# Optimization experiments

Measured on AMD Instinct MI355X. Metric: run time of the kernel, lower is better.

Reference implementation:

```python
import jax, jax.numpy as jnp
import numpy as np

N = 4096
DIMS = {"word": 768, "pos": 64, "liwc": 93, "entity": 256, "text": 768}
HID, OUT = 256, 128
VIEWS = ["word", "pos", "liwc", "entity", "text"]


def setup_inputs() -> dict:
    key = jax.random.key(0)
    inp = {}
    for i, v in enumerate(VIEWS):
        ka, kx, k1, k2 = jax.random.split(jax.random.fold_in(key, i), 4)
        d = DIMS[v]
        # dense row-normalized adjacency surrogate
        a = jax.random.uniform(ka, (N, N), dtype=jnp.float32)
        inp[f"adj_{v}"] = a / jnp.sum(a, axis=1, keepdims=True)
        inp[f"x_{v}"] = jax.random.normal(kx, (N, d), dtype=jnp.float32)
        inp[f"W1_{v}"] = jax.random.normal(k1, (d, HID), dtype=jnp.float32) * (2.0 / (d + HID)) ** 0.5
        inp[f"b1_{v}"] = jnp.zeros((HID,), dtype=jnp.float32)
        inp[f"W2_{v}"] = jax.random.normal(k2, (HID, OUT), dtype=jnp.float32) * (2.0 / (HID + OUT)) ** 0.5
        inp[f"b2_{v}"] = jnp.zeros((OUT,), dtype=jnp.float32)
    return inp


def _gcn2(adj, x, W1, b1, W2, b2):
    # layer 1: adj @ (x @ W1) + b1, relu (dropout is identity in eval mode)
    h = jax.nn.relu(adj @ (x @ W1) + b1)
    # layer 2
    return adj @ (h @ W2) + b2


def reference(adj_word, adj_pos, adj_liwc, adj_entity, adj_text,
              x_word, x_pos, x_liwc, x_entity, x_text,
              W1_word, b1_word, W2_word, b2_word,
              W1_pos, b1_pos, W2_pos, b2_pos,
              W1_liwc, b1_liwc, W2_liwc, b2_liwc,
              W1_entity, b1_entity, W2_entity, b2_entity,
              W1_text, b1_text, W2_text, b2_text):
    return (
        _gcn2(adj_word, x_word, W1_word, b1_word, W2_word, b2_word),
        _gcn2(adj_pos, x_pos, W1_pos, b1_pos, W2_pos, b2_pos),
        _gcn2(adj_liwc, x_liwc, W1_liwc, b1_liwc, W2_liwc, b2_liwc),
        _gcn2(adj_entity, x_entity, W1_entity, b1_entity, W2_entity, b2_entity),
        _gcn2(adj_text, x_text, W1_text, b1_text, W2_text, b2_text),
    )
```

## Files before the change

kernel.cpp:

```cpp
#include <hip/hip_runtime.h>
#include <stdint.h>

typedef unsigned short u16;
typedef __attribute__((ext_vector_type(8))) __bf16 bf16x8;
typedef __attribute__((ext_vector_type(4))) float f32x4;
typedef __attribute__((ext_vector_type(4))) u16 u16x4;
typedef __attribute__((ext_vector_type(8))) u16 u16x8;

#define BM 128
#define BN 128
#define BK 32
#define MTOT 4096

__device__ __forceinline__ u16 f2bf(float f) {
  union { float f; uint32_t u; } x; x.f = f;
  uint32_t r = x.u + 0x7FFFu + ((x.u >> 16) & 1u);
  return (u16)(r >> 16);
}
__device__ __forceinline__ float bf2f(u16 h) {
  union { uint32_t u; float f; } x; x.u = ((uint32_t)h) << 16;
  return x.f;
}

__device__ __forceinline__ void gload16(const void* g, void* lds) {
  __builtin_amdgcn_global_load_lds(
      (const __attribute__((address_space(1))) void*)g,
      (__attribute__((address_space(3))) void*)lds, 16, 0, 0);
}

struct ViewParams {
  const void* A;
  const u16* BT;
  void* C;
  const float* bias;
  int ldab, lda, N;
  int kspan;
  size_t partStride;
};
struct Params5 { ViewParams v[5]; };

template <int FLAGS, bool AF32, bool CF32>
__global__ __launch_bounds__(256) void gemm_kernel(Params5 p, int tilesPerView,
                                                   int ntiles, int kchunks) {
  constexpr int ABYTES = AF32 ? (BM * BK * 4) : (BM * BK * 2);
  constexpr int BUFB = ABYTES + BN * BK * 2;
  __shared__ __align__(16) char smem[2 * BUFB];

  const int bid = blockIdx.x;
  const int view = bid / tilesPerView;
  const int t = bid - view * tilesPerView;
  const int kc = t % kchunks;
  const int t2 = t / kchunks;
  const int nt = t2 % ntiles;
  const int mt = t2 / ntiles;
  ViewParams vp = p.v[view];
  const int ldab = vp.ldab, lda = vp.lda, N = vp.N;
  const int m0 = mt * BM, n0 = nt * BN;
  const int kbase = kc * vp.kspan;

  const int tid = threadIdx.x;
  const int wave = tid >> 6;
  const int lane = tid & 63;

  const int srow = lane >> 2;
  const int slot4 = lane & 3;
  const int rB0 = wave * 32 + srow;
  const int rB1 = rB0 + 16;
  const int cB0 = slot4 ^ ((rB0 >> 1) & 3);
  const int cB1 = slot4 ^ ((rB1 >> 1) & 3);
  const u16* gB0 = vp.BT + (size_t)(n0 + rB0) * ldab + kbase + cB0 * 8;
  const u16* gB1 = vp.BT + (size_t)(n0 + rB1) * ldab + kbase + cB1 * 8;
  const int lB0_off = ABYTES + (wave * 32) * 32 * 2;
  const int lB1_off = ABYTES + (wave * 32 + 16) * 32 * 2;

  const float* gAf[4];
  const u16 *gAb0 = nullptr, *gAb1 = nullptr;
  int lA_off[4];
  if constexpr (AF32) {
    const float* Af = (const float*)vp.A;
    const int arow = lane >> 3;
    const int slot8 = lane & 7;
#pragma unroll
    for (int i = 0; i < 4; i++) {
      int r = wave * 32 + i * 8 + arow;
      int c = slot8 ^ (r & 7);
      gAf[i] = Af + (size_t)(m0 + r) * lda + kbase + c * 4;
      lA_off[i] = (wave * 32 + i * 8) * 32 * 4;
    }
  } else {
    const u16* Ab = (const u16*)vp.A;
    const int rA0 = wave * 32 + srow;
    const int rA1 = rA0 + 16;
    const int cA0 = slot4 ^ ((rA0 >> 1) & 3);
    const int cA1 = slot4 ^ ((rA1 >> 1) & 3);
    gAb0 = Ab + (size_t)(m0 + rA0) * lda + kbase + cA0 * 8;
    gAb1 = Ab + (size_t)(m0 + rA1) * lda + kbase + cA1 * 8;
    lA_off[0] = (wave * 32) * 32 * 2;
    lA_off[1] = (wave * 32 + 16) * 32 * 2;
  }

  const int lm = lane & 15;
  const int q = lane >> 4;
  const int wm = (wave >> 1) * 64;
  const int wn = (wave & 1) * 64;
  int aoff0[4], aoff1[4], boff[4];
#pragma unroll
  for (int i = 0; i < 4; i++) {
    int ml = wm + i * 16 + lm;
    if constexpr (AF32) {
      aoff0[i] = ml * 32 + ((2 * q) ^ (ml & 7)) * 4;
      aoff1[i] = ml * 32 + ((2 * q + 1) ^ (ml & 7)) * 4;
    } else {
      aoff0[i] = ml * 32 + (q ^ ((ml >> 1) & 3)) * 8;
    }
    int nl = wn + i * 16 + lm;
    boff[i] = nl * 32 + (q ^ ((nl >> 1) & 3)) * 8;
  }

  f32x4 acc[4][4];
#pragma unroll
  for (int i = 0; i < 4; i++)
#pragma unroll
    for (int j = 0; j < 4; j++) acc[i][j] = 0.0f;

  auto stage = [&](char* bufp) {
    if constexpr (AF32) {
#pragma unroll
      for (int i = 0; i < 4; i++) { gload16(gAf[i], bufp + lA_off[i]); gAf[i] += BK; }
    } else {
      gload16(gAb0, bufp + lA_off[0]);
      gload16(gAb1, bufp + lA_off[1]);
      gAb0 += BK; gAb1 += BK;
    }
    gload16(gB0, bufp + lB0_off);
    gload16(gB1, bufp + lB1_off);
    gB0 += BK; gB1 += BK;
  };

  auto compute = [&](const char* bufp) {
    bf16x8 af[4], bfr[4];
#pragma unroll
    for (int i = 0; i < 4; i++) {
      if constexpr (AF32) {
        f32x4 lo = *(const f32x4*)((const float*)bufp + aoff0[i]);
        f32x4 hi = *(const f32x4*)((const float*)bufp + aoff1[i]);
        bf16x8 a;
#pragma unroll
        for (int tt = 0; tt < 4; tt++) { a[tt] = (__bf16)lo[tt]; a[tt + 4] = (__bf16)hi[tt]; }
        af[i] = a;
      } else {
        af[i] = *(const bf16x8*)((const u16*)bufp + aoff0[i]);
      }
    }
    const u16* Bs = (const u16*)(bufp + ABYTES);
#pragma unroll
    for (int j = 0; j < 4; j++) bfr[j] = *(const bf16x8*)(Bs + boff[j]);
#pragma unroll
    for (int i = 0; i < 4; i++)
#pragma unroll
      for (int j = 0; j < 4; j++)
        acc[i][j] = __builtin_amdgcn_mfma_f32_16x16x32_bf16(af[i], bfr[j], acc[i][j], 0, 0, 0);
  };

  char* curp = smem;
  char* nxtp = smem + BUFB;
  stage(curp);
  __syncthreads();
  const int nsteps = vp.kspan / BK;
  for (int s = 0; s < nsteps - 1; s++) {
    stage(nxtp);
    compute(curp);
    __syncthreads();
    char* tmp = curp; curp = nxtp; nxtp = tmp;
  }
  compute(curp);

#pragma unroll
  for (int j = 0; j < 4; j++) {
    const int n = n0 + wn + j * 16 + lm;
    float bv = 0.0f;
    if (FLAGS & 2) bv = vp.bias[n];
#pragma unroll
    for (int i = 0; i < 4; i++) {
      const int mb = m0 + wm + i * 16 + q * 4;
      float v0 = acc[i][j][0], v1 = acc[i][j][1], v2 = acc[i][j][2], v3 = acc[i][j][3];
      if (FLAGS & 2) { v0 += bv; v1 += bv; v2 += bv; v3 += bv; }
      if (FLAGS & 4) {
        v0 = fmaxf(v0, 0.0f); v1 = fmaxf(v1, 0.0f);
        v2 = fmaxf(v2, 0.0f); v3 = fmaxf(v3, 0.0f);
      }
      if constexpr ((FLAGS & 1) != 0) {
        u16x4 pk;
        pk[0] = f2bf(v0); pk[1] = f2bf(v1); pk[2] = f2bf(v2); pk[3] = f2bf(v3);
        *(u16x4*)((u16*)vp.C + (size_t)kc * vp.partStride + (size_t)n * MTOT + mb) = pk;
      } else if constexpr (CF32) {
        float* cp = (float*)vp.C + (size_t)kc * vp.partStride + (size_t)mb * N + n;
        cp[0] = v0; cp[N] = v1; cp[2 * N] = v2; cp[3 * N] = v3;
      } else {
        u16* cp = (u16*)vp.C + (size_t)kc * vp.partStride + (size_t)mb * N + n;
        cp[0] = f2bf(v0); cp[N] = f2bf(v1); cp[2 * N] = f2bf(v2); cp[3 * N] = f2bf(v3);
      }
    }
  }
}

struct CombParams { const u16* parts; u16* out; const float* b[5]; int kchunks; };
__global__ __launch_bounds__(256) void comb_h_kernel(CombParams cp) {
  int idx = blockIdx.x * 256 + threadIdx.x;
  int v = idx >> 17;
  int e = (idx & 131071) << 3;
  float acc[8] = {0, 0, 0, 0, 0, 0, 0, 0};
  for (int kc = 0; kc < cp.kchunks; kc++) {
    u16x8 t = *(const u16x8*)(cp.parts + (((size_t)(kc * 5 + v)) << 20) + e);
#pragma unroll
    for (int j = 0; j < 8; j++) acc[j] += bf2f(t[j]);
  }
  const float* bp = cp.b[v] + (e & 255);
  u16x8 o;
#pragma unroll
  for (int j = 0; j < 8; j++) o[j] = f2bf(fmaxf(acc[j] + bp[j], 0.0f));
  *(u16x8*)(cp.out + (((size_t)v) << 20) + e) = o;
}

struct CombFParams { const float* parts; float* out; const float* b[5]; int kchunks; };
__global__ __launch_bounds__(256) void combf_kernel(CombFParams cp) {
  int idx = blockIdx.x * 256 + threadIdx.x;
  int v = idx >> 16;
  int e = (idx & 65535) << 3;
  float acc[8] = {0, 0, 0, 0, 0, 0, 0, 0};
  for (int kc = 0; kc < cp.kchunks; kc++) {
    const float* pp = cp.parts + (((size_t)(kc * 5 + v)) << 19) + e;
    f32x4 a = *(const f32x4*)pp;
    f32x4 b = *(const f32x4*)(pp + 4);
#pragma unroll
    for (int j = 0; j < 4; j++) { acc[j] += a[j]; acc[j + 4] += b[j]; }
  }
  const float* bp = cp.b[v] + (e & 127);
  f32x4 o0, o1;
#pragma unroll
  for (int j = 0; j < 4; j++) { o0[j] = acc[j] + bp[j]; o1[j] = acc[j + 4] + bp[j + 4]; }
  float* op = cp.out + (((size_t)v) << 19) + e;
  *(f32x4*)op = o0;
  *(f32x4*)(op + 4) = o1;
}

struct PrepParams {
  const float* W1[5]; u16* W1T[5];
  const float* W2[5]; u16* W2T[5];
  const float* xl; float* xlp;
  int d[5]; int Kp[5];
};

__global__ void prep_kernel(PrepParams p, int total) {
  int idx = blockIdx.x * 256 + threadIdx.x;
  if (idx >= total) return;
  int off = 0;
#pragma unroll
  for (int v = 0; v < 5; v++) {
    int sz = 256 * p.Kp[v];
    if (idx < off + sz) {
      int r = idx - off;
      int n = r / p.Kp[v];
      int k = r - n * p.Kp[v];
      p.W1T[v][r] = (k < p.d[v]) ? f2bf(p.W1[v][(size_t)k * 256 + n]) : (u16)0;
      return;
    }
    off += sz;
  }
#pragma unroll
  for (int v = 0; v < 5; v++) {
    if (idx < off + 128 * 256) {
      int r = idx - off;
      int n = r >> 8, k = r & 255;
      p.W2T[v][r] = f2bf(p.W2[v][(size_t)k * 128 + n]);
      return;
    }
    off += 128 * 256;
  }
  {
    int r = idx - off;
    int m = r / 96, k = r - m * 96;
    p.xlp[r] = (k < 93) ? p.xl[(size_t)m * 93 + k] : 0.0f;
  }
}

extern "C" void kernel_launch(void* const* d_in, const int* in_sizes, int n_in,
                              void* d_out, int out_size, void* d_ws, size_t ws_size,
                              hipStream_t stream) {
  (void)in_sizes; (void)n_in; (void)out_size;
  static const int dims[5] = {768, 64, 93, 256, 768};
  static const int Kp[5]   = {768, 64, 96, 256, 768};

  const float *adjf[5], *xf[5], *W1f[5], *b1f[5], *W2f[5], *b2f[5];
  for (int v = 0; v < 5; v++) {
    adjf[v] = (const float*)d_in[6 * v + 0];
    xf[v]   = (const float*)d_in[6 * v + 1];
    W1f[v]  = (const float*)d_in[6 * v + 2];
    b1f[v]  = (const float*)d_in[6 * v + 3];
    W2f[v]  = (const float*)d_in[6 * v + 4];
    b2f[v]  = (const float*)d_in[6 * v + 5];
  }

  const size_t VIEW = (size_t)256 * 4096;
  const size_t TV   = (size_t)128 * 4096;
  char* ws = (char*)d_ws;
  size_t off = 0;
  auto carve = [&](size_t bytes) { char* pp = ws + off; off += (bytes + 15) & ~(size_t)15; return pp; };
  u16* W1T[5]; for (int v = 0; v < 5; v++) W1T[v] = (u16*)carve((size_t)256 * Kp[v] * 2);
  u16* W2T[5]; for (int v = 0; v < 5; v++) W2T[v] = (u16*)carve((size_t)128 * 256 * 2);
  float* xlp = (float*)carve((size_t)4096 * 96 * 4);
  u16* Y1T = (u16*)carve(5 * VIEW * 2);
  u16* PARTS = (u16*)carve(2 * 5 * VIEW * 2);
  u16* HT = (u16*)carve(5 * VIEW * 2);
  const bool ksplit = ws_size >= off;
  u16* TT = Y1T;
  float* PARTSF = (float*)PARTS;

  PrepParams pp;
  int prepTot = 0;
  for (int v = 0; v < 5; v++) {
    pp.W1[v] = W1f[v]; pp.W1T[v] = W1T[v];
    pp.W2[v] = W2f[v]; pp.W2T[v] = W2T[v];
    pp.d[v] = dims[v]; pp.Kp[v] = Kp[v];
    prepTot += 256 * Kp[v];
  }
  pp.xl = xf[2]; pp.xlp = xlp;
  prepTot += 5 * 128 * 256 + 4096 * 96;
  prep_kernel<<<(prepTot + 255) / 256, 256, 0, stream>>>(pp, prepTot);

  Params5 pa;
  for (int v = 0; v < 5; v++)
    pa.v[v] = ViewParams{ (v == 2 ? (const void*)xlp : (const void*)xf[v]), W1T[v], Y1T + v * VIEW,
                          nullptr, Kp[v], Kp[v], 256, Kp[v], 0 };
  gemm_kernel<1, true, false><<<320, 256, 0, stream>>>(pa, 64, 2, 1);

  if (ksplit) {
    Params5 pb;
    for (int v = 0; v < 5; v++)
      pb.v[v] = ViewParams{ adjf[v], Y1T + v * VIEW, PARTS + v * VIEW,
                            nullptr, 4096, 4096, 256, 2048, 5 * VIEW };
    gemm_kernel<0, true, false><<<640, 256, 0, stream>>>(pb, 128, 2, 2);

    CombParams c1{ PARTS, HT, { b1f[0], b1f[1], b1f[2], b1f[3], b1f[4] }, 2 };
    comb_h_kernel<<<2560, 256, 0, stream>>>(c1);

    Params5 pc;
    for (int v = 0; v < 5; v++)
      pc.v[v] = ViewParams{ HT + v * VIEW, W2T[v], TT + v * TV,
                            nullptr, 256, 256, 128, 256, 0 };
    gemm_kernel<1, false, false><<<160, 256, 0, stream>>>(pc, 32, 1, 1);

    Params5 pd;
    for (int v = 0; v < 5; v++)
      pd.v[v] = ViewParams{ adjf[v], TT + v * TV, PARTSF + v * TV,
                            nullptr, 4096, 4096, 128, 2048, 5 * TV };
    gemm_kernel<0, true, true><<<320, 256, 0, stream>>>(pd, 64, 1, 2);

    CombFParams c2{ PARTSF, (float*)d_out, { b2f[0], b2f[1], b2f[2], b2f[3], b2f[4] }, 2 };
    combf_kernel<<<1280, 256, 0, stream>>>(c2);
  } else {
    Params5 pb;
    for (int v = 0; v < 5; v++)
      pb.v[v] = ViewParams{ adjf[v], Y1T + v * VIEW, HT + v * VIEW,
                            b1f[v], 4096, 4096, 256, 4096, 0 };
    gemm_kernel<6, true, false><<<320, 256, 0, stream>>>(pb, 64, 2, 1);

    Params5 pc;
    for (int v = 0; v < 5; v++)
      pc.v[v] = ViewParams{ HT + v * VIEW, W2T[v], TT + v * TV,
                            nullptr, 256, 256, 128, 256, 0 };
    gemm_kernel<1, false, false><<<160, 256, 0, stream>>>(pc, 32, 1, 1);

    Params5 pd;
    float* outp = (float*)d_out;
    for (int v = 0; v < 5; v++)
      pd.v[v] = ViewParams{ adjf[v], TT + v * TV, outp + v * TV,
                            b2f[v], 4096, 4096, 128, 4096, 0 };
    gemm_kernel<2, true, true><<<160, 256, 0, stream>>>(pd, 32, 1, 1);
  }
}
```

Baseline: 574.2 us.

## Triple-buffer GEMM K-loop with vmcnt waits and raise second adj GEMM split-K

Replaces the double-buffered LDS pipeline with a three-stage ring that keeps two tile loads in flight, using explicit s_waitcnt vmcnt counts and raw barriers instead of __syncthreads. The aim is to hide global-load latency of the large fp32 adjacency reads. The layer-2 adjacency GEMM also moves from 2-way to 4-way split-K (640 blocks) for better CU occupancy, which enlarges the partial-sum workspace and the final combine reads. LDS use per block grows by half, which may reduce occupancy, and the hardcoded vmcnt counts must match the per-stage load instruction count.

```diff
diff --git a/kernel.cpp b/kernel.cpp
--- a/kernel.cpp
+++ b/kernel.cpp
@@ -26,6 +26,11 @@
   __builtin_amdgcn_global_load_lds(
       (const __attribute__((address_space(1))) void*)g,
       (__attribute__((address_space(3))) void*)lds, 16, 0, 0);
+}
+
+template <int N>
+__device__ __forceinline__ void wait_vmcnt() {
+  asm volatile("s_waitcnt vmcnt(%0)" ::"n"(N) : "memory");
 }
 
 struct ViewParams {
@@ -44,7 +49,8 @@
                                                    int ntiles, int kchunks) {
   constexpr int ABYTES = AF32 ? (BM * BK * 4) : (BM * BK * 2);
   constexpr int BUFB = ABYTES + BN * BK * 2;
-  __shared__ __align__(16) char smem[2 * BUFB];
+  constexpr int LPS = AF32 ? 6 : 4;
+  __shared__ __align__(16) char smem[3 * BUFB];
 
   const int bid = blockIdx.x;
   const int view = bid / tilesPerView;
@@ -162,18 +168,28 @@
         acc[i][j] = __builtin_amdgcn_mfma_f32_16x16x32_bf16(af[i], bfr[j], acc[i][j], 0, 0, 0);
   };
 
-  char* curp = smem;
-  char* nxtp = smem + BUFB;
-  stage(curp);
-  __syncthreads();
   const int nsteps = vp.kspan / BK;
-  for (int s = 0; s < nsteps - 1; s++) {
-    stage(nxtp);
-    compute(curp);
-    __syncthreads();
-    char* tmp = curp; curp = nxtp; nxtp = tmp;
-  }
-  compute(curp);
+  char* b0 = smem;
+  char* b1 = smem + BUFB;
+  char* b2 = smem + 2 * BUFB;
+  stage(b0);
+  if (nsteps > 1) stage(b1);
+  if (nsteps > 2) stage(b2);
+
+  for (int s = 0; s < nsteps; s++) {
+    const int rem = nsteps - 1 - s;
+    if (rem >= 2)      wait_vmcnt<2 * LPS>();
+    else if (rem == 1) wait_vmcnt<LPS>();
+    else               wait_vmcnt<0>();
+    __builtin_amdgcn_s_barrier();
+    compute(b0);
+    if (rem >= 3) {
+      asm volatile("" ::: "memory");
+      __builtin_amdgcn_s_barrier();
+      stage(b0);
+    }
+    char* tmp = b0; b0 = b1; b1 = b2; b2 = tmp;
+  }
 
 #pragma unroll
   for (int j = 0; j < 4; j++) {
@@ -310,7 +326,7 @@
   u16* W2T[5]; for (int v = 0; v < 5; v++) W2T[v] = (u16*)carve((size_t)128 * 256 * 2);
   float* xlp = (float*)carve((size_t)4096 * 96 * 4);
   u16* Y1T = (u16*)carve(5 * VIEW * 2);
-  u16* PARTS = (u16*)carve(2 * 5 * VIEW * 2);
+  u16* PARTS = (u16*)carve((size_t)4 * 5 * TV * 4);
   u16* HT = (u16*)carve(5 * VIEW * 2);
   const bool ksplit = ws_size >= off;
   u16* TT = Y1T;
@@ -353,10 +369,10 @@
     Params5 pd;
     for (int v = 0; v < 5; v++)
       pd.v[v] = ViewParams{ adjf[v], TT + v * TV, PARTSF + v * TV,
-                            nullptr, 4096, 4096, 128, 2048, 5 * TV };
-    gemm_kernel<0, true, true><<<320, 256, 0, stream>>>(pd, 64, 1, 2);
-
-    CombFParams c2{ PARTSF, (float*)d_out, { b2f[0], b2f[1], b2f[2], b2f[3], b2f[4] }, 2 };
+                            nullptr, 4096, 4096, 128, 1024, 5 * TV };
+    gemm_kernel<0, true, true><<<640, 256, 0, stream>>>(pd, 128, 1, 4);
+
+    CombFParams c2{ PARTSF, (float*)d_out, { b2f[0], b2f[1], b2f[2], b2f[3], b2f[4] }, 4 };
     combf_kernel<<<1280, 256, 0, stream>>>(c2);
   } else {
     Params5 pb;
```

Measured after the change: 564.1 us. No clear change (-1.8%).
